# Kernel tuning notes

Measured on AMD Instinct MI355X. Metric: run time of the kernel, lower is better.

The kernel has to match this reference:

```python
import jax, jax.numpy as jnp
from jax import lax
import numpy as np

B, T, IN, H, OUT = 8192, 512, 8, 64, 1


def setup_inputs() -> dict:
    key = jax.random.key(0)
    ks = jax.random.split(key, 7)
    s_ih = 1.0 / np.sqrt(H)
    # PyTorch LSTM param layout: gates stacked as [i, f, g, o] along dim 0
    W_ih = jax.random.uniform(ks[0], (4 * H, IN), jnp.float32, -s_ih, s_ih)
    W_hh = jax.random.uniform(ks[1], (4 * H, H), jnp.float32, -s_ih, s_ih)
    b_ih = jax.random.uniform(ks[2], (4 * H,), jnp.float32, -s_ih, s_ih)
    b_hh = jax.random.uniform(ks[3], (4 * H,), jnp.float32, -s_ih, s_ih)
    W_fc = jax.random.uniform(ks[4], (OUT, H), jnp.float32, -s_ih, s_ih)
    b_fc = jax.random.uniform(ks[5], (OUT,), jnp.float32, -s_ih, s_ih)
    x = jax.random.normal(ks[6], (B, T, IN), jnp.float32)
    return {"x": x, "W_ih": W_ih, "W_hh": W_hh, "b_ih": b_ih,
            "b_hh": b_hh, "W_fc": W_fc, "b_fc": b_fc}


def _lstm_last_h(x, W_ih, W_hh, b_ih, b_hh):
    # x: [B, T, IN] -> last hidden state [B, H]
    Bn = x.shape[0]
    Hn = W_hh.shape[1]
    b = b_ih + b_hh  # [4H]

    def step(carry, xt):
        h, c = carry  # [B, H] each
        gates = xt @ W_ih.T + h @ W_hh.T + b  # [B, 4H]
        i, f, g, o = jnp.split(gates, 4, axis=-1)
        i = jax.nn.sigmoid(i)
        f = jax.nn.sigmoid(f)
        g = jnp.tanh(g)
        o = jax.nn.sigmoid(o)
        c = f * c + i * g
        h = o * jnp.tanh(c)
        return (h, c), None

    h0 = jnp.zeros((Bn, Hn), x.dtype)
    c0 = jnp.zeros((Bn, Hn), x.dtype)
    (hT, _), _ = lax.scan(step, (h0, c0), jnp.swapaxes(x, 0, 1))  # scan over T
    return hT


def reference(x, W_ih, W_hh, b_ih, b_hh, W_fc, b_fc):
    hT = _lstm_last_h(x, W_ih, W_hh, b_ih, b_hh)  # [B, H]
    return hT @ W_fc.T + b_fc  # [B, OUT]
```

## Files before the change

### kernel.cpp

```cpp
#include <hip/hip_runtime.h>


typedef _Float16 f16_t;
typedef _Float16 half8 __attribute__((ext_vector_type(8)));
typedef _Float16 half4 __attribute__((ext_vector_type(4)));
typedef __fp16 fp16x2 __attribute__((ext_vector_type(2)));
typedef float floatx2 __attribute__((ext_vector_type(2)));
typedef float floatx4 __attribute__((ext_vector_type(4)));

#define Bn 8192
#define Tn 512
#define INn 8
#define Hn 64
#define BT 16
#define CHUNK 16
#define NCHUNK (Tn / CHUNK)
#define HSTRIDE 72
#define XROW 24

__device__ __forceinline__ floatx2 act_pair(float zi0, float zi1,
                                            float zf0, float zf1,
                                            float zg0, float zg1,
                                            float zo0, float zo1,
                                            floatx2& chat) {
  const floatx2 one  = {1.f, 1.f};
  const float  K2   = 2.8853900817779268f;
  const floatx2 K2v  = {K2, K2};
  const floatx2 mK2v = {-K2, -K2};
  const floatx2 clmp = {126.f, 126.f};
  floatx2 A = {__builtin_amdgcn_exp2f(zi0), __builtin_amdgcn_exp2f(zi1)};
  floatx2 G = {__builtin_amdgcn_exp2f(zg0), __builtin_amdgcn_exp2f(zg1)};
  floatx2 F = {__builtin_amdgcn_exp2f(zf0), __builtin_amdgcn_exp2f(zf1)};
  floatx2 O = {__builtin_amdgcn_exp2f(zo0), __builtin_amdgcn_exp2f(zo1)};
  floatx2 PA  = A + one;
  floatx2 PG  = G + one;
  floatx2 PF  = F + one;
  floatx2 PAG = PA * PG;
  floatx2 num = __builtin_elementwise_fma(G, K2v, mK2v) * PF;
  floatx2 s   = __builtin_elementwise_fma(chat, PAG, num);
  floatx2 P3  = PF * PAG;
  floatx2 R   = {__builtin_amdgcn_rcpf(P3.x), __builtin_amdgcn_rcpf(P3.y)};
  chat = __builtin_elementwise_min(s * R, clmp);
  floatx2 C2 = {__builtin_amdgcn_exp2f(chat.x), __builtin_amdgcn_exp2f(chat.y)};
  floatx2 P4 = (O + one) * (C2 + one);
  floatx2 Rh = {__builtin_amdgcn_rcpf(P4.x), __builtin_amdgcn_rcpf(P4.y)};
  return (C2 - one) * Rh;
}

__global__ __launch_bounds__(256, 2)
void lstm_fused(const float* __restrict__ xg,
                const float* __restrict__ W_ih,
                const float* __restrict__ W_hh,
                const float* __restrict__ b_ih,
                const float* __restrict__ b_hh,
                const float* __restrict__ W_fc,
                const float* __restrict__ b_fc,
                float* __restrict__ out)
{
  __shared__ alignas(16) f16_t hbuf[2][BT][HSTRIDE];
  __shared__ alignas(16) f16_t xlds[2][CHUNK][BT][XROW];

  const int tid   = threadIdx.x;
  const int wv    = tid >> 6;
  const int lane  = tid & 63;
  const int n     = lane & 15;
  const int q     = lane >> 4;
  const int bbase = blockIdx.x * BT;

  const float LOG2E = 1.4426950408889634f;

  half8 bf[4][2];
  half4 bfx[4];
  #pragma unroll
  for (int g = 0; g < 4; ++g) {
    const float sc = (g == 2) ? (2.f * LOG2E) : (-LOG2E);
    const int C = g * 64 + wv * 16 + n;
    #pragma unroll
    for (int c = 0; c < 2; ++c) {
      half8 v;
      #pragma unroll
      for (int j = 0; j < 8; ++j) {
        const int k = c * 32 + q * 8 + j;
        v[j] = (f16_t)(W_hh[C * Hn + k] * sc);
      }
      bf[g][c] = v;
    }
    half4 vx;
    #pragma unroll
    for (int j = 0; j < 4; ++j) {
      const int k = q * 4 + j;
      vx[j] = (f16_t)((k < INn) ? (W_ih[C * INn + k] * sc) : 0.f);
    }
    bfx[g] = vx;
  }

  const int u0 = wv * 16 + q * 4;
  floatx4 bi, bfv, bg, bo;
  #pragma unroll
  for (int r = 0; r < 4; ++r) {
    const int uu = u0 + r;
    bi[r]  = -(b_ih[uu]        + b_hh[uu])        * LOG2E;
    bfv[r] = -(b_ih[64 + uu]   + b_hh[64 + uu])   * LOG2E;
    bg[r]  =  (b_ih[128 + uu]  + b_hh[128 + uu])  * (2.f * LOG2E);
    bo[r]  = -(b_ih[192 + uu]  + b_hh[192 + uu])  * LOG2E;
  }

  for (int i = tid; i < BT * HSTRIDE; i += 256) ((f16_t*)hbuf[0])[i] = (f16_t)0.f;
  for (int i = tid; i < 2 * CHUNK * BT * XROW; i += 256) ((f16_t*)xlds)[i] = (f16_t)0.f;
  __syncthreads();

  const int row_s = tid >> 4;
  const int tt_s  = tid & 15;
  const float* xps = xg + ((size_t)(bbase + row_s) * Tn + tt_s) * INn;

  float4 pa = *(const float4*)(xps);
  float4 pb2 = *(const float4*)(xps + 4);

  floatx2 chat01 = {0.f, 0.f};
  floatx2 chat23 = {0.f, 0.f};

  for (int ch = 0; ch < NCHUNK; ++ch) {
    union { half8 v; fp16x2 h2[4]; } P;
    P.h2[0] = __builtin_amdgcn_cvt_pkrtz(pa.x, pa.y);
    P.h2[1] = __builtin_amdgcn_cvt_pkrtz(pa.z, pa.w);
    P.h2[2] = __builtin_amdgcn_cvt_pkrtz(pb2.x, pb2.y);
    P.h2[3] = __builtin_amdgcn_cvt_pkrtz(pb2.z, pb2.w);
    *(half8*)&xlds[ch & 1][tt_s][row_s][0] = P.v;
    __syncthreads();

    const int chn = (ch + 1 < NCHUNK) ? (ch + 1) : 0;
    pa  = *(const float4*)(xps + (size_t)chn * CHUNK * INn);
    pb2 = *(const float4*)(xps + (size_t)chn * CHUNK * INn + 4);

    #pragma unroll
    for (int tt = 0; tt < CHUNK; ++tt) {
      const int p  = tt & 1;
      const int pn = p ^ 1;

      const half8 b0 = *(const half8*)&hbuf[p][n][q * 8];
      const half8 b1 = *(const half8*)&hbuf[p][n][32 + q * 8];
      const half4 bx = *(const half4*)&xlds[ch & 1][tt][n][q * 4];

      floatx4 ai = __builtin_amdgcn_mfma_f32_16x16x32_f16(bf[0][0], b0, bi,  0, 0, 0);
      floatx4 af = __builtin_amdgcn_mfma_f32_16x16x32_f16(bf[1][0], b0, bfv, 0, 0, 0);
      floatx4 ag = __builtin_amdgcn_mfma_f32_16x16x32_f16(bf[2][0], b0, bg,  0, 0, 0);
      floatx4 ao = __builtin_amdgcn_mfma_f32_16x16x32_f16(bf[3][0], b0, bo,  0, 0, 0);
      ai = __builtin_amdgcn_mfma_f32_16x16x32_f16(bf[0][1], b1, ai, 0, 0, 0);
      af = __builtin_amdgcn_mfma_f32_16x16x32_f16(bf[1][1], b1, af, 0, 0, 0);
      ag = __builtin_amdgcn_mfma_f32_16x16x32_f16(bf[2][1], b1, ag, 0, 0, 0);
      ao = __builtin_amdgcn_mfma_f32_16x16x32_f16(bf[3][1], b1, ao, 0, 0, 0);
      ai = __builtin_amdgcn_mfma_f32_16x16x16f16(bfx[0], bx, ai, 0, 0, 0);
      af = __builtin_amdgcn_mfma_f32_16x16x16f16(bfx[1], bx, af, 0, 0, 0);
      ag = __builtin_amdgcn_mfma_f32_16x16x16f16(bfx[2], bx, ag, 0, 0, 0);
      ao = __builtin_amdgcn_mfma_f32_16x16x16f16(bfx[3], bx, ao, 0, 0, 0);

      const floatx2 h01 = act_pair(ai[0], ai[1], af[0], af[1],
                                   ag[0], ag[1], ao[0], ao[1], chat01);
      const floatx2 h23 = act_pair(ai[2], ai[3], af[2], af[3],
                                   ag[2], ag[3], ao[2], ao[3], chat23);

      union { half4 v; fp16x2 h2[2]; } Wq;
      Wq.h2[0] = __builtin_amdgcn_cvt_pkrtz(h01.x, h01.y);
      Wq.h2[1] = __builtin_amdgcn_cvt_pkrtz(h23.x, h23.y);
      *(half4*)&hbuf[pn][n][u0] = Wq.v;

      __syncthreads();
    }
  }

  if (tid < 64) {
    const int b = lane & 15;
    const int part = lane >> 4;
    float s = 0.f;
    #pragma unroll
    for (int k = 0; k < 16; ++k) {
      const int uu = part * 16 + k;
      s = __builtin_fmaf((float)hbuf[0][b][uu], W_fc[uu], s);
    }
    s += __shfl_down(s, 32);
    s += __shfl_down(s, 16);
    if (lane < 16) out[bbase + b] = s + b_fc[0];
  }
}

extern "C" void kernel_launch(void* const* d_in, const int* in_sizes, int n_in,
                              void* d_out, int out_size, void* d_ws, size_t ws_size,
                              hipStream_t stream) {
  const float* x    = (const float*)d_in[0];
  const float* W_ih = (const float*)d_in[1];
  const float* W_hh = (const float*)d_in[2];
  const float* b_ih = (const float*)d_in[3];
  const float* b_hh = (const float*)d_in[4];
  const float* W_fc = (const float*)d_in[5];
  const float* b_fc = (const float*)d_in[6];
  float* out = (float*)d_out;
  dim3 grid(Bn / BT), block(256);
  hipLaunchKernelGGL(lstm_fused, grid, block, 0, stream,
                     x, W_ih, W_hh, b_ih, b_hh, W_fc, b_fc, out);
}
```

Baseline: 446.0 us.

## Overlap x-chunk staging with recurrence and drop per-chunk barrier

Moves the write of the next x chunk into LDS inside the timestep loop, just after the MFMAs of step 0, and moves the global prefetch two chunks ahead. This removes the separate per-chunk __syncthreads by relying on the existing per-step barriers. It also preloads all 16 x fragments for a chunk into registers and raises wave priority around the MFMA block. In exchange, register pressure goes up, and correctness depends on the double-buffer ordering across the per-step barriers.

```diff
diff --git a/kernel.cpp b/kernel.cpp
--- a/kernel.cpp
+++ b/kernel.cpp
@@ -105,32 +105,43 @@
     bo[r]  = -(b_ih[192 + uu]  + b_hh[192 + uu])  * LOG2E;
   }
 
-  for (int i = tid; i < BT * HSTRIDE; i += 256) ((f16_t*)hbuf[0])[i] = (f16_t)0.f;
-  for (int i = tid; i < 2 * CHUNK * BT * XROW; i += 256) ((f16_t*)xlds)[i] = (f16_t)0.f;
-  __syncthreads();
-
   const int row_s = tid >> 4;
   const int tt_s  = tid & 15;
   const float* xps = xg + ((size_t)(bbase + row_s) * Tn + tt_s) * INn;
 
-  float4 pa = *(const float4*)(xps);
-  float4 pb2 = *(const float4*)(xps + 4);
+  for (int i = tid; i < BT * HSTRIDE; i += 256) ((f16_t*)hbuf[0])[i] = (f16_t)0.f;
+  {
+    const half8 z = {};
+    #pragma unroll
+    for (int r = tid; r < 2 * CHUNK * BT; r += 256) {
+      f16_t* base = &xlds[r >> 8][(r >> 4) & 15][r & 15][0];
+      *(half8*)(base + 8)  = z;
+      *(half8*)(base + 16) = z;
+    }
+  }
+  {
+    float4 a  = *(const float4*)(xps);
+    float4 b2 = *(const float4*)(xps + 4);
+    union { half8 v; fp16x2 h2[4]; } P;
+    P.h2[0] = __builtin_amdgcn_cvt_pkrtz(a.x, a.y);
+    P.h2[1] = __builtin_amdgcn_cvt_pkrtz(a.z, a.w);
+    P.h2[2] = __builtin_amdgcn_cvt_pkrtz(b2.x, b2.y);
+    P.h2[3] = __builtin_amdgcn_cvt_pkrtz(b2.z, b2.w);
+    *(half8*)&xlds[0][tt_s][row_s][0] = P.v;
+  }
+  float4 pa  = *(const float4*)(xps + CHUNK * INn);
+  float4 pb2 = *(const float4*)(xps + CHUNK * INn + 4);
+
+  __syncthreads();
 
   floatx2 chat01 = {0.f, 0.f};
   floatx2 chat23 = {0.f, 0.f};
 
   for (int ch = 0; ch < NCHUNK; ++ch) {
-    union { half8 v; fp16x2 h2[4]; } P;
-    P.h2[0] = __builtin_amdgcn_cvt_pkrtz(pa.x, pa.y);
-    P.h2[1] = __builtin_amdgcn_cvt_pkrtz(pa.z, pa.w);
-    P.h2[2] = __builtin_amdgcn_cvt_pkrtz(pb2.x, pb2.y);
-    P.h2[3] = __builtin_amdgcn_cvt_pkrtz(pb2.z, pb2.w);
-    *(half8*)&xlds[ch & 1][tt_s][row_s][0] = P.v;
-    __syncthreads();
-
-    const int chn = (ch + 1 < NCHUNK) ? (ch + 1) : 0;
-    pa  = *(const float4*)(xps + (size_t)chn * CHUNK * INn);
-    pb2 = *(const float4*)(xps + (size_t)chn * CHUNK * INn + 4);
+    half4 bx[CHUNK];
+    #pragma unroll
+    for (int t = 0; t < CHUNK; ++t)
+      bx[t] = *(const half4*)&xlds[ch & 1][t][n][q * 4];
 
     #pragma unroll
     for (int tt = 0; tt < CHUNK; ++tt) {
@@ -139,8 +150,8 @@
 
       const half8 b0 = *(const half8*)&hbuf[p][n][q * 8];
       const half8 b1 = *(const half8*)&hbuf[p][n][32 + q * 8];
-      const half4 bx = *(const half4*)&xlds[ch & 1][tt][n][q * 4];
-
+
+      __builtin_amdgcn_s_setprio(1);
       floatx4 ai = __builtin_amdgcn_mfma_f32_16x16x32_f16(bf[0][0], b0, bi,  0, 0, 0);
       floatx4 af = __builtin_amdgcn_mfma_f32_16x16x32_f16(bf[1][0], b0, bfv, 0, 0, 0);
       floatx4 ag = __builtin_amdgcn_mfma_f32_16x16x32_f16(bf[2][0], b0, bg,  0, 0, 0);
@@ -149,10 +160,25 @@
       af = __builtin_amdgcn_mfma_f32_16x16x32_f16(bf[1][1], b1, af, 0, 0, 0);
       ag = __builtin_amdgcn_mfma_f32_16x16x32_f16(bf[2][1], b1, ag, 0, 0, 0);
       ao = __builtin_amdgcn_mfma_f32_16x16x32_f16(bf[3][1], b1, ao, 0, 0, 0);
-      ai = __builtin_amdgcn_mfma_f32_16x16x16f16(bfx[0], bx, ai, 0, 0, 0);
-      af = __builtin_amdgcn_mfma_f32_16x16x16f16(bfx[1], bx, af, 0, 0, 0);
-      ag = __builtin_amdgcn_mfma_f32_16x16x16f16(bfx[2], bx, ag, 0, 0, 0);
-      ao = __builtin_amdgcn_mfma_f32_16x16x16f16(bfx[3], bx, ao, 0, 0, 0);
+      ai = __builtin_amdgcn_mfma_f32_16x16x16f16(bfx[0], bx[tt], ai, 0, 0, 0);
+      af = __builtin_amdgcn_mfma_f32_16x16x16f16(bfx[1], bx[tt], af, 0, 0, 0);
+      ag = __builtin_amdgcn_mfma_f32_16x16x16f16(bfx[2], bx[tt], ag, 0, 0, 0);
+      ao = __builtin_amdgcn_mfma_f32_16x16x16f16(bfx[3], bx[tt], ao, 0, 0, 0);
+      __builtin_amdgcn_s_setprio(0);
+
+      if (tt == 0) {
+        union { half8 v; fp16x2 h2[4]; } P;
+        P.h2[0] = __builtin_amdgcn_cvt_pkrtz(pa.x, pa.y);
+        P.h2[1] = __builtin_amdgcn_cvt_pkrtz(pa.z, pa.w);
+        P.h2[2] = __builtin_amdgcn_cvt_pkrtz(pb2.x, pb2.y);
+        P.h2[3] = __builtin_amdgcn_cvt_pkrtz(pb2.z, pb2.w);
+        *(half8*)&xlds[(ch + 1) & 1][tt_s][row_s][0] = P.v;
+      }
+      if (tt == 1) {
+        const int chn = (ch + 2 < NCHUNK) ? (ch + 2) : (ch + 2 - NCHUNK);
+        pa  = *(const float4*)(xps + (size_t)chn * CHUNK * INn);
+        pb2 = *(const float4*)(xps + (size_t)chn * CHUNK * INn + 4);
+      }
 
       const floatx2 h01 = act_pair(ai[0], ai[1], af[0], af[1],
                                    ag[0], ag[1], ao[0], ao[1], chat01);
```

Result: no change. 438.0 us, median of 2 (-1.8%).
